# Performance work log

Hardware: AMD Instinct MI355X
Metric: run time of the kernel (lower is better)

## Reference

```python
import jax, jax.numpy as jnp
import numpy as np

N, L, HOP = 512, 16, 8  # L // 2


def overlap_and_add(frames, hop):
    # frames: [..., K, L] -> [..., (K-1)*hop + L]
    K, Lf = frames.shape[-2], frames.shape[-1]
    T = (K - 1) * hop + Lf
    idx = (jnp.arange(K)[:, None] * hop + jnp.arange(Lf)[None, :]).reshape(-1)
    flat = frames.reshape(frames.shape[:-2] + (K * Lf,))
    out = jnp.zeros(frames.shape[:-2] + (T,), frames.dtype)
    return out.at[..., idx].add(flat)


def setup_inputs() -> dict:
    key = jax.random.key(0)
    k1, k2, k3 = jax.random.split(key, 3)
    M, C, K = 8, 2, 6000
    inputs = jax.random.normal(k1, (M, N, K), dtype=jnp.float32)
    est_mask = jax.random.uniform(k2, (M, C, N, K), dtype=jnp.float32)
    W = jax.random.normal(k3, (N, L), dtype=jnp.float32) * 0.05
    return {"inputs": inputs, "est_mask": est_mask, "W": W}


def reference(inputs, est_mask, W):
    # masked source spectra: [M, C, N, K]
    masked = inputs[:, None, :, :] * est_mask
    # transpose to [M, C, K, N] and project N -> L (fused in einsum)
    frames = jnp.einsum('mcnk,nl->mckl', masked, W)  # [M, C, K, L]
    # overlap-and-add with hop L // 2 -> [M, C, T]
    return overlap_and_add(frames, HOP)
```

## Files before the change

kernel.cpp:

```cpp
#include <hip/hip_runtime.h>

#define NN   512
#define LL   16
#define MM   8
#define CC   2
#define KK   6000
#define TT   ((KK - 1) * 8 + 16)
#define KW   64
#define NCH  32
#define NC   (NN / NCH)
#define ROWB (KK * 4)
#define TENS_B (NCH * KW * 4)
#define BUF_B  (3 * TENS_B)

typedef __attribute__((address_space(3))) void       lds_v;
typedef __attribute__((address_space(1))) const void glob_v;

__global__ __launch_bounds__(512, 6) void decoder_dma_kernel(
    const float* __restrict__ inputs,
    const float* __restrict__ est_mask,
    const float* __restrict__ W,
    float* __restrict__ out)
{
    __shared__ __align__(16) char lds[2 * BUF_B];

    const int tid = threadIdx.x;
    const int t   = tid & 63;
    const int wq  = __builtin_amdgcn_readfirstlane(tid >> 6);
    const int kb  = blockIdx.x;
    const int m   = blockIdx.y;

    const int lane_r = t >> 4;
    int cb = kb * 256 + (t & 15) * 16;
    if (cb > ROWB - 16) cb = ROWB - 16;
    const size_t lane_off = (size_t)lane_r * ROWB + cb;

    const char* tb0 = (const char*)inputs   + (size_t)m * NN * ROWB;
    const char* tb1 = (const char*)est_mask + (size_t)(m * CC) * NN * ROWB;
    const char* tb2 = tb1 + (size_t)NN * ROWB;

    char* dst_base = lds + wq * 1024;

    auto issue = [&](int c, int bsel) {
        const size_t rowoff = (size_t)(c * NCH + wq * 4) * ROWB + lane_off;
        char* bb = dst_base + bsel * BUF_B;
        __builtin_amdgcn_global_load_lds((glob_v*)(tb0 + rowoff), (lds_v*)(bb),              16, 0, 0);
        __builtin_amdgcn_global_load_lds((glob_v*)(tb1 + rowoff), (lds_v*)(bb + TENS_B),     16, 0, 0);
        __builtin_amdgcn_global_load_lds((glob_v*)(tb2 + rowoff), (lds_v*)(bb + 2 * TENS_B), 16, 0, 0);
    };

    float acc0[LL], acc1[LL];
    #pragma unroll
    for (int l = 0; l < LL; ++l) { acc0[l] = 0.f; acc1[l] = 0.f; }

    issue(0, 0);

    for (int c = 0; c < NC; ++c) {
        if (c + 1 < NC) {
            issue(c + 1, (c + 1) & 1);
            asm volatile("s_waitcnt vmcnt(3)" ::: "memory");
        } else {
            asm volatile("s_waitcnt vmcnt(0)" ::: "memory");
        }
        __builtin_amdgcn_sched_barrier(0);

        const float* Lb = (const float*)(lds + (c & 1) * BUF_B + wq * 1024);

        #pragma unroll
        for (int rr = 0; rr < 4; ++rr) {
            const int n = c * NCH + wq * 4 + rr;
            float wv[LL];
            *reinterpret_cast<float4*>(&wv[0])  = *(const float4*)(W + n * LL + 0);
            *reinterpret_cast<float4*>(&wv[4])  = *(const float4*)(W + n * LL + 4);
            *reinterpret_cast<float4*>(&wv[8])  = *(const float4*)(W + n * LL + 8);
            *reinterpret_cast<float4*>(&wv[12]) = *(const float4*)(W + n * LL + 12);

            const float xin = Lb[rr * 64 + t];
            const float xm0 = Lb[(TENS_B / 4) + rr * 64 + t];
            const float xm1 = Lb[(2 * TENS_B / 4) + rr * 64 + t];
            const float x0 = xin * xm0;
            const float x1 = xin * xm1;
            #pragma unroll
            for (int l = 0; l < LL; ++l) {
                acc0[l] = fmaf(x0, wv[l], acc0[l]);
                acc1[l] = fmaf(x1, wv[l], acc1[l]);
            }
        }
    }

    __syncthreads();

    float* sm = (float*)lds;
    if (wq >= 4) {
        float* d = &sm[((wq - 4) * 64 + t) * 33];
        #pragma unroll
        for (int l = 0; l < LL; ++l) { d[l] = acc0[l]; d[16 + l] = acc1[l]; }
    }
    __syncthreads();
    if (wq < 4) {
        const float* s = &sm[(wq * 64 + t) * 33];
        #pragma unroll
        for (int l = 0; l < LL; ++l) { acc0[l] += s[l]; acc1[l] += s[16 + l]; }
    }
    __syncthreads();
    if (wq == 2 || wq == 3) {
        float* d = &sm[((wq - 2) * 64 + t) * 33];
        #pragma unroll
        for (int l = 0; l < LL; ++l) { d[l] = acc0[l]; d[16 + l] = acc1[l]; }
    }
    __syncthreads();
    if (wq < 2) {
        const float* s = &sm[(wq * 64 + t) * 33];
        #pragma unroll
        for (int l = 0; l < LL; ++l) { acc0[l] += s[l]; acc1[l] += s[16 + l]; }
    }
    __syncthreads();
    if (wq == 1) {
        float* d = &sm[t * 33];
        #pragma unroll
        for (int l = 0; l < LL; ++l) { d[l] = acc0[l]; d[16 + l] = acc1[l]; }
    }
    __syncthreads();

    if (wq == 0) {
        {
            const float* s = &sm[t * 33];
            #pragma unroll
            for (int l = 0; l < LL; ++l) { acc0[l] += s[l]; acc1[l] += s[16 + l]; }
        }

        const int k = kb * KW + t;
        float ph0[8], ph1[8];
        #pragma unroll
        for (int j = 0; j < 8; ++j) {
            ph0[j] = __shfl_up(acc0[8 + j], 1);
            ph1[j] = __shfl_up(acc1[8 + j], 1);
        }

        if (k < KK) {
            float* o0 = out + ((size_t)m * CC + 0) * TT + 8 * k;
            float* o1 = out + ((size_t)m * CC + 1) * TT + 8 * k;

            if (t == 0) {
                #pragma unroll
                for (int j = 0; j < 8; ++j) {
                    atomicAdd(&o0[j], acc0[j]);
                    atomicAdd(&o1[j], acc1[j]);
                }
            } else {
                #pragma unroll
                for (int j = 0; j < 8; ++j) {
                    o0[j] = acc0[j] + ph0[j];
                    o1[j] = acc1[j] + ph1[j];
                }
            }
            if (t == 63 || k == KK - 1) {
                #pragma unroll
                for (int j = 0; j < 8; ++j) {
                    atomicAdd(&o0[8 + j], acc0[8 + j]);
                    atomicAdd(&o1[8 + j], acc1[8 + j]);
                }
            }
        }
    }
}

extern "C" void kernel_launch(void* const* d_in, const int* in_sizes, int n_in,
                              void* d_out, int out_size, void* d_ws, size_t ws_size,
                              hipStream_t stream) {
    const float* inputs   = (const float*)d_in[0];
    const float* est_mask = (const float*)d_in[1];
    const float* W        = (const float*)d_in[2];
    float*       out      = (float*)d_out;

    hipMemsetAsync(out, 0, (size_t)out_size * sizeof(float), stream);

    dim3 grid((KK + KW - 1) / KW, MM);
    decoder_dma_kernel<<<grid, 512, 0, stream>>>(inputs, est_mask, W, out);
}
```

Measured before the change: 65.24 us.

## Widen K tile to two frames per lane and remap blocks across XCDs

Each lane now handles two adjacent frames, read as float2 from LDS, so every W row load feeds twice as many FMAs. The N chunk is halved to keep the LDS footprint the same. Blocks are flattened into a 1D grid and remapped so each XCD gets a contiguous set of K tiles, which should improve L2 locality. Adjacent frame pairs are overlap-added in registers, which cuts down on shuffles and atomics. In exchange register pressure goes up (launch bounds drop to 4), there are fewer blocks (47x8), and the cross-wave reduction needs extra LDS passes.

New measurement: 58.94 us (median of 3 runs). 9.7% less time.

```diff
diff --git a/kernel.cpp b/kernel.cpp
--- a/kernel.cpp
+++ b/kernel.cpp
@@ -6,8 +6,10 @@
 #define CC   2
 #define KK   6000
 #define TT   ((KK - 1) * 8 + 16)
-#define KW   64
-#define NCH  32
+#define KW   128
+#define NKB  47
+#define NKBP 48
+#define NCH  16
 #define NC   (NN / NCH)
 #define ROWB (KK * 4)
 #define TENS_B (NCH * KW * 4)
@@ -16,7 +18,7 @@
 typedef __attribute__((address_space(3))) void       lds_v;
 typedef __attribute__((address_space(1))) const void glob_v;
 
-__global__ __launch_bounds__(512, 6) void decoder_dma_kernel(
+__global__ __launch_bounds__(512, 4) void decoder_dma_kernel(
     const float* __restrict__ inputs,
     const float* __restrict__ est_mask,
     const float* __restrict__ W,
@@ -24,14 +26,19 @@
 {
     __shared__ __align__(16) char lds[2 * BUF_B];
 
+    const int bid = blockIdx.x;
+    const int xcd = bid & 7;
+    const int s   = bid >> 3;
+    const int kb  = xcd * 6 + (s % 6);
+    const int m   = s / 6;
+    if (kb >= NKB) return;
+
     const int tid = threadIdx.x;
     const int t   = tid & 63;
     const int wq  = __builtin_amdgcn_readfirstlane(tid >> 6);
-    const int kb  = blockIdx.x;
-    const int m   = blockIdx.y;
-
-    const int lane_r = t >> 4;
-    int cb = kb * 256 + (t & 15) * 16;
+
+    const int lane_r = t >> 5;
+    int cb = kb * 512 + (t & 31) * 16;
     if (cb > ROWB - 16) cb = ROWB - 16;
     const size_t lane_off = (size_t)lane_r * ROWB + cb;
 
@@ -42,16 +49,16 @@
     char* dst_base = lds + wq * 1024;
 
     auto issue = [&](int c, int bsel) {
-        const size_t rowoff = (size_t)(c * NCH + wq * 4) * ROWB + lane_off;
+        const size_t rowoff = (size_t)(c * NCH + wq * 2) * ROWB + lane_off;
         char* bb = dst_base + bsel * BUF_B;
         __builtin_amdgcn_global_load_lds((glob_v*)(tb0 + rowoff), (lds_v*)(bb),              16, 0, 0);
         __builtin_amdgcn_global_load_lds((glob_v*)(tb1 + rowoff), (lds_v*)(bb + TENS_B),     16, 0, 0);
         __builtin_amdgcn_global_load_lds((glob_v*)(tb2 + rowoff), (lds_v*)(bb + 2 * TENS_B), 16, 0, 0);
     };
 
-    float acc0[LL], acc1[LL];
+    float a0A[LL], a0B[LL], a1A[LL], a1B[LL];
     #pragma unroll
-    for (int l = 0; l < LL; ++l) { acc0[l] = 0.f; acc1[l] = 0.f; }
+    for (int l = 0; l < LL; ++l) { a0A[l] = 0.f; a0B[l] = 0.f; a1A[l] = 0.f; a1B[l] = 0.f; }
 
     issue(0, 0);
 
@@ -64,26 +71,28 @@
         }
         __builtin_amdgcn_sched_barrier(0);
 
-        const float* Lb = (const float*)(lds + (c & 1) * BUF_B + wq * 1024);
-
-        #pragma unroll
-        for (int rr = 0; rr < 4; ++rr) {
-            const int n = c * NCH + wq * 4 + rr;
+        const char* Lb = lds + (c & 1) * BUF_B + wq * 1024;
+
+        #pragma unroll
+        for (int r = 0; r < 2; ++r) {
+            const int n = c * NCH + wq * 2 + r;
             float wv[LL];
             *reinterpret_cast<float4*>(&wv[0])  = *(const float4*)(W + n * LL + 0);
             *reinterpret_cast<float4*>(&wv[4])  = *(const float4*)(W + n * LL + 4);
             *reinterpret_cast<float4*>(&wv[8])  = *(const float4*)(W + n * LL + 8);
             *reinterpret_cast<float4*>(&wv[12]) = *(const float4*)(W + n * LL + 12);
 
-            const float xin = Lb[rr * 64 + t];
-            const float xm0 = Lb[(TENS_B / 4) + rr * 64 + t];
-            const float xm1 = Lb[(2 * TENS_B / 4) + rr * 64 + t];
-            const float x0 = xin * xm0;
-            const float x1 = xin * xm1;
+            const float2 vin = reinterpret_cast<const float2*>(Lb + r * 512)[t];
+            const float2 vm0 = reinterpret_cast<const float2*>(Lb + TENS_B + r * 512)[t];
+            const float2 vm1 = reinterpret_cast<const float2*>(Lb + 2 * TENS_B + r * 512)[t];
+            const float x0A = vin.x * vm0.x, x0B = vin.y * vm0.y;
+            const float x1A = vin.x * vm1.x, x1B = vin.y * vm1.y;
             #pragma unroll
             for (int l = 0; l < LL; ++l) {
-                acc0[l] = fmaf(x0, wv[l], acc0[l]);
-                acc1[l] = fmaf(x1, wv[l], acc1[l]);
+                a0A[l] = fmaf(x0A, wv[l], a0A[l]);
+                a0B[l] = fmaf(x0B, wv[l], a0B[l]);
+                a1A[l] = fmaf(x1A, wv[l], a1A[l]);
+                a1B[l] = fmaf(x1B, wv[l], a1B[l]);
             }
         }
     }
@@ -94,71 +103,101 @@
     if (wq >= 4) {
         float* d = &sm[((wq - 4) * 64 + t) * 33];
         #pragma unroll
-        for (int l = 0; l < LL; ++l) { d[l] = acc0[l]; d[16 + l] = acc1[l]; }
+        for (int l = 0; l < LL; ++l) { d[l] = a0A[l]; d[16 + l] = a0B[l]; }
     }
     __syncthreads();
     if (wq < 4) {
-        const float* s = &sm[(wq * 64 + t) * 33];
-        #pragma unroll
-        for (int l = 0; l < LL; ++l) { acc0[l] += s[l]; acc1[l] += s[16 + l]; }
+        const float* sp = &sm[(wq * 64 + t) * 33];
+        #pragma unroll
+        for (int l = 0; l < LL; ++l) { a0A[l] += sp[l]; a0B[l] += sp[16 + l]; }
+    }
+    __syncthreads();
+    if (wq >= 4) {
+        float* d = &sm[((wq - 4) * 64 + t) * 33];
+        #pragma unroll
+        for (int l = 0; l < LL; ++l) { d[l] = a1A[l]; d[16 + l] = a1B[l]; }
+    }
+    __syncthreads();
+    if (wq < 4) {
+        const float* sp = &sm[(wq * 64 + t) * 33];
+        #pragma unroll
+        for (int l = 0; l < LL; ++l) { a1A[l] += sp[l]; a1B[l] += sp[16 + l]; }
     }
     __syncthreads();
     if (wq == 2 || wq == 3) {
-        float* d = &sm[((wq - 2) * 64 + t) * 33];
-        #pragma unroll
-        for (int l = 0; l < LL; ++l) { d[l] = acc0[l]; d[16 + l] = acc1[l]; }
+        float* d = &sm[((wq - 2) * 64 + t) * 67];
+        #pragma unroll
+        for (int l = 0; l < LL; ++l) {
+            d[l] = a0A[l]; d[16 + l] = a0B[l];
+            d[32 + l] = a1A[l]; d[48 + l] = a1B[l];
+        }
     }
     __syncthreads();
     if (wq < 2) {
-        const float* s = &sm[(wq * 64 + t) * 33];
-        #pragma unroll
-        for (int l = 0; l < LL; ++l) { acc0[l] += s[l]; acc1[l] += s[16 + l]; }
+        const float* sp = &sm[(wq * 64 + t) * 67];
+        #pragma unroll
+        for (int l = 0; l < LL; ++l) {
+            a0A[l] += sp[l]; a0B[l] += sp[16 + l];
+            a1A[l] += sp[32 + l]; a1B[l] += sp[48 + l];
+        }
     }
     __syncthreads();
     if (wq == 1) {
-        float* d = &sm[t * 33];
-        #pragma unroll
-        for (int l = 0; l < LL; ++l) { d[l] = acc0[l]; d[16 + l] = acc1[l]; }
+        float* d = &sm[t * 67];
+        #pragma unroll
+        for (int l = 0; l < LL; ++l) {
+            d[l] = a0A[l]; d[16 + l] = a0B[l];
+            d[32 + l] = a1A[l]; d[48 + l] = a1B[l];
+        }
     }
     __syncthreads();
 
     if (wq == 0) {
         {
-            const float* s = &sm[t * 33];
+            const float* sp = &sm[t * 67];
             #pragma unroll
-            for (int l = 0; l < LL; ++l) { acc0[l] += s[l]; acc1[l] += s[16 + l]; }
-        }
-
-        const int k = kb * KW + t;
+            for (int l = 0; l < LL; ++l) {
+                a0A[l] += sp[l]; a0B[l] += sp[16 + l];
+                a1A[l] += sp[32 + l]; a1B[l] += sp[48 + l];
+            }
+        }
+
+        const int kA = kb * KW + 2 * t;
         float ph0[8], ph1[8];
         #pragma unroll
         for (int j = 0; j < 8; ++j) {
-            ph0[j] = __shfl_up(acc0[8 + j], 1);
-            ph1[j] = __shfl_up(acc1[8 + j], 1);
-        }
-
-        if (k < KK) {
-            float* o0 = out + ((size_t)m * CC + 0) * TT + 8 * k;
-            float* o1 = out + ((size_t)m * CC + 1) * TT + 8 * k;
+            ph0[j] = __shfl_up(a0B[8 + j], 1);
+            ph1[j] = __shfl_up(a1B[8 + j], 1);
+        }
+
+        if (kA < KK) {
+            float* o0 = out + ((size_t)m * CC + 0) * TT + 8 * kA;
+            float* o1 = out + ((size_t)m * CC + 1) * TT + 8 * kA;
 
             if (t == 0) {
                 #pragma unroll
                 for (int j = 0; j < 8; ++j) {
-                    atomicAdd(&o0[j], acc0[j]);
-                    atomicAdd(&o1[j], acc1[j]);
+                    atomicAdd(&o0[j], a0A[j]);
+                    atomicAdd(&o1[j], a1A[j]);
                 }
             } else {
                 #pragma unroll
                 for (int j = 0; j < 8; ++j) {
-                    o0[j] = acc0[j] + ph0[j];
-                    o1[j] = acc1[j] + ph1[j];
+                    o0[j] = a0A[j] + ph0[j];
+                    o1[j] = a1A[j] + ph1[j];
                 }
             }
-            if (t == 63 || k == KK - 1) {
+            #pragma unroll
+            for (int j = 0; j < 8; ++j) {
+                o0[8 + j] = a0B[j] + a0A[8 + j];
+                o1[8 + j] = a1B[j] + a1A[8 + j];
+            }
+            const int kB = kA + 1;
+            if (t == 63 || kB == KK - 1) {
                 #pragma unroll
                 for (int j = 0; j < 8; ++j) {
-                    atomicAdd(&o0[8 + j], acc0[8 + j]);
-                    atomicAdd(&o1[8 + j], acc1[8 + j]);
+                    atomicAdd(&o0[16 + j], a0B[8 + j]);
+                    atomicAdd(&o1[16 + j], a1B[8 + j]);
                 }
             }
         }
@@ -175,6 +214,5 @@
 
     hipMemsetAsync(out, 0, (size_t)out_size * sizeof(float), stream);
 
-    dim3 grid((KK + KW - 1) / KW, MM);
-    decoder_dma_kernel<<<grid, 512, 0, stream>>>(inputs, est_mask, W, out);
+    decoder_dma_kernel<<<dim3(NKBP * MM), 512, 0, stream>>>(inputs, est_mask, W, out);
 }
```
